# Kernel tuning notes

Hardware: AMD Instinct MI355X
Metric: run time of the kernel (lower is better)

The kernel has to match this reference:

```python
import jax, jax.numpy as jnp
import numpy as np

N = 100000
E = 1600000
D = 128  # in_dim == out_dim


def setup_inputs() -> dict:
    key = jax.random.key(0)
    k1, k2, k3, k4, k5 = jax.random.split(key, 5)
    x = jax.random.normal(k1, (N, D), dtype=jnp.float32)
    edge_index = jax.random.randint(k2, (2, E), 0, N, dtype=jnp.int64)
    edge_attr = jax.random.normal(k3, (E, 8), dtype=jnp.float32)
    # nn.Linear(in_dim, out_dim) params: W [out, in], b [out]
    bound = 1.0 / np.sqrt(D)
    W = jax.random.uniform(k4, (D, D), minval=-bound, maxval=bound, dtype=jnp.float32)
    b = jax.random.uniform(k5, (D,), minval=-bound, maxval=bound, dtype=jnp.float32)
    return {"x": x, "edge_index": edge_index, "edge_attr": edge_attr, "W": W, "b": b}


def reference(x, edge_index, edge_attr, W, b):
    row, col = edge_index[0], edge_index[1]
    # gather neighbor features then scatter-add into destination rows
    agg = jax.ops.segment_sum(x[col], row, num_segments=x.shape[0])  # [N, D]
    h = (x + agg) @ W.T + b  # linear
    return jax.nn.silu(h)
```

## Files before the change

kernel.cpp:

```cpp
#include <hip/hip_runtime.h>
#include <math.h>

#define NN 100000
#define NE 1600000
#define DD 128
#define CAP 64

#define NB     64
#define CHUNK  25000
#define NBUCK  800
#define BNODES 125
#define QCAP2  56
#define OVCAP  8192

typedef short bf16x8 __attribute__((ext_vector_type(8)));
typedef float f32x4  __attribute__((ext_vector_type(4)));

__device__ inline float bf2f(unsigned short u) {
    unsigned int v = ((unsigned int)u) << 16;
    return __uint_as_float(v);
}
__device__ inline unsigned short f2bf(float f) {
    unsigned int u = __float_as_uint(f);
    unsigned int r = (u + 0x7FFFu + ((u >> 16) & 1u)) >> 16;
    return (unsigned short)r;
}

__global__ void f2bf_kernel(const float* __restrict__ src,
                            unsigned short* __restrict__ dst, int n4) {
    int i = blockIdx.x * blockDim.x + threadIdx.x;
    if (i >= n4) return;
    float4 v = ((const float4*)src)[i];
    ushort4 o;
    o.x = f2bf(v.x); o.y = f2bf(v.y); o.z = f2bf(v.z); o.w = f2bf(v.w);
    ((ushort4*)dst)[i] = o;
}

__global__ void zero_ovn_kernel(int* ovn) { *ovn = 0; }

__global__ __launch_bounds__(256)
void partition_kernel(const int* __restrict__ eidx,
                      unsigned long long* __restrict__ q,
                      int* __restrict__ qn,
                      unsigned long long* __restrict__ ovf,
                      int* __restrict__ ovn) {
    __shared__ int qc[NBUCK];
    for (int i = threadIdx.x; i < NBUCK; i += 256) qc[i] = 0;
    __syncthreads();
    const int base = blockIdx.x * CHUNK;
    for (int i = threadIdx.x; i < CHUNK; i += 256) {
        const int e = base + i;
        const int r = __builtin_nontemporal_load(&eidx[e]);
        const int c = __builtin_nontemporal_load(&eidx[NE + e]);
        const int b = r / BNODES;
        const int pos = atomicAdd(&qc[b], 1);
        const unsigned long long pk =
            ((unsigned long long)(unsigned)c << 32) | (unsigned)r;
        if (pos < QCAP2) {
            q[((size_t)blockIdx.x * NBUCK + b) * QCAP2 + pos] = pk;
        } else {
            const int op = atomicAdd(ovn, 1);
            if (op < OVCAP) ovf[op] = pk;
        }
    }
    __syncthreads();
    for (int i = threadIdx.x; i < NBUCK; i += 256) {
        int v = qc[i]; if (v > QCAP2) v = QCAP2;
        qn[blockIdx.x * NBUCK + i] = v;
    }
}

__global__ __launch_bounds__(512)
void build_gather_kernel(const unsigned short* __restrict__ x16,
                         const unsigned long long* __restrict__ q,
                         const int* __restrict__ qn,
                         const unsigned long long* __restrict__ ovf,
                         const int* __restrict__ ovn,
                         unsigned short* __restrict__ V16) {
    __shared__ __align__(16) int adj_l[BNODES * CAP];
    __shared__ int cnt_l[BNODES];
    const int g   = blockIdx.x;
    const int lo  = g * BNODES;
    const int tid = threadIdx.x;

    for (int i = tid; i < BNODES; i += 512) cnt_l[i] = 0;
    __syncthreads();

    {
        const int p   = tid >> 3;
        const int sub = tid & 7;
        const int n = qn[p * NBUCK + g];
        const unsigned long long* qq = q + ((size_t)p * NBUCK + g) * QCAP2;
        for (int i = sub; i < n; i += 8) {
            const unsigned long long pk = qq[i];
            const int r = (int)(pk & 0xffffffffu) - lo;
            const int c = (int)(pk >> 32);
            const int pos = atomicAdd(&cnt_l[r], 1);
            if (pos < CAP) adj_l[(r << 6) + pos] = c;
        }
    }
    {
        int n = *ovn; if (n > OVCAP) n = OVCAP;
        for (int i = tid; i < n; i += 512) {
            const unsigned long long pk = ovf[i];
            const int r = (int)(pk & 0xffffffffu) - lo;
            if ((unsigned)r < (unsigned)BNODES) {
                const int c = (int)(pk >> 32);
                const int pos = atomicAdd(&cnt_l[r], 1);
                if (pos < CAP) adj_l[(r << 6) + pos] = c;
            }
        }
    }
    __syncthreads();

    const int lane = tid & 15;
    const bf16x8* xv = (const bf16x8*)x16;
    for (int ni = (tid >> 4); ni < BNODES; ni += 32) {
        const int node = lo + ni;

        bf16x8 s = xv[(size_t)node * 16 + lane];
        float a[8];
        #pragma unroll
        for (int k = 0; k < 8; ++k) a[k] = bf2f((unsigned short)s[k]);

        int deg = cnt_l[ni]; if (deg > CAP) deg = CAP;
        const int* arow = &adj_l[ni << 6];

        for (int d = 0; d < deg; d += 8) {
            const int4 c0 = *(const int4*)&arow[d];
            const int4 c1 = *(const int4*)&arow[d + 4];
            int idx[8] = {c0.x, c0.y, c0.z, c0.w, c1.x, c1.y, c1.z, c1.w};
            float w[8];
            #pragma unroll
            for (int j = 0; j < 8; ++j) {
                const bool live = (d + j) < deg;
                w[j] = live ? 1.f : 0.f;
                if (!live) idx[j] = node;
            }
            bf16x8 t[8];
            #pragma unroll
            for (int j = 0; j < 8; ++j) t[j] = xv[(size_t)idx[j] * 16 + lane];
            #pragma unroll
            for (int j = 0; j < 8; ++j) {
                #pragma unroll
                for (int k = 0; k < 8; ++k)
                    a[k] = fmaf(w[j], bf2f((unsigned short)t[j][k]), a[k]);
            }
        }

        bf16x8 o;
        #pragma unroll
        for (int k = 0; k < 8; ++k) o[k] = (short)f2bf(a[k]);
        ((bf16x8*)V16)[(size_t)node * 16 + lane] = o;
    }
}

__global__ __launch_bounds__(256)
void gemm_mfma_kernel(const unsigned short* __restrict__ V16,
                      const unsigned short* __restrict__ W16,
                      const float* __restrict__ bias,
                      float* __restrict__ out) {
    const int wave = threadIdx.x >> 6;
    const int lane = threadIdx.x & 63;
    const int strip = blockIdx.x * 4 + wave;
    if (strip >= NN / 16) return;
    const int m0 = strip << 4;
    const int r = lane & 15;
    const int q = lane >> 4;

    const bf16x8* Arow = (const bf16x8*)(V16 + (size_t)(m0 + r) * 128);
    bf16x8 a[4];
    #pragma unroll
    for (int kk = 0; kk < 4; ++kk) a[kk] = Arow[kk * 4 + q];

    f32x4 acc[8];
    #pragma unroll
    for (int n = 0; n < 8; ++n) acc[n] = (f32x4){0.f, 0.f, 0.f, 0.f};

    #pragma unroll
    for (int kk = 0; kk < 4; ++kk) {
        #pragma unroll
        for (int n = 0; n < 8; ++n) {
            const bf16x8 b =
                ((const bf16x8*)(W16 + (size_t)(n * 16 + r) * 128))[kk * 4 + q];
            acc[n] = __builtin_amdgcn_mfma_f32_16x16x32_bf16(a[kk], b, acc[n], 0, 0, 0);
        }
    }

    #pragma unroll
    for (int n = 0; n < 8; ++n) {
        const int col = n * 16 + r;
        const float bv = bias[col];
        #pragma unroll
        for (int i = 0; i < 4; ++i) {
            const int row = m0 + q * 4 + i;
            float h = acc[n][i] + bv;
            h = h / (1.f + __expf(-h));
            out[(size_t)row * 128 + col] = h;
        }
    }
}

extern "C" void kernel_launch(void* const* d_in, const int* in_sizes, int n_in,
                              void* d_out, int out_size, void* d_ws, size_t ws_size,
                              hipStream_t stream) {
    const float* x    = (const float*)d_in[0];
    const int*   eidx = (const int*)d_in[1];
    const float* W    = (const float*)d_in[3];
    const float* b    = (const float*)d_in[4];
    float* out = (float*)d_out;

    char* ws = (char*)d_ws;
    int*                qn  = (int*)ws;
    int*                ovn = (int*)(ws + (256u << 10));
    unsigned long long* ovf = (unsigned long long*)(ws + (320u << 10));
    unsigned long long* q   = (unsigned long long*)(ws + (512u << 10));
    unsigned short*     x16 = (unsigned short*)(ws + (26u << 20));
    unsigned short*     V16 = (unsigned short*)(ws + (51u << 20));
    unsigned short*     W16 = (unsigned short*)(ws + (76u << 20));

    zero_ovn_kernel<<<1, 1, 0, stream>>>(ovn);
    partition_kernel<<<NB, 256, 0, stream>>>(eidx, q, qn, ovf, ovn);
    f2bf_kernel<<<(NN * DD / 4 + 255) / 256, 256, 0, stream>>>(x, x16, NN * DD / 4);
    f2bf_kernel<<<(DD * DD / 4 + 255) / 256, 256, 0, stream>>>(W, W16, DD * DD / 4);
    build_gather_kernel<<<NBUCK, 512, 0, stream>>>(x16, q, qn, ovf, ovn, V16);
    gemm_mfma_kernel<<<(NN / 16 + 3) / 4, 256, 0, stream>>>(V16, W16, b, out);
}
```

Before: 311.9 us.

## Fuse neighbor gather with MFMA GEMM via LDS and merge prep kernels

The aggregation result for each 128-node bucket is written into shared memory with an XOR swizzle instead of global memory. The same block then runs the bf16 MFMA linear plus SiLU on it, which removes the V16 global round trip and a separate GEMM launch. The partition and bf16 conversions are merged into a single prep kernel, and the counter reset becomes a memset. Buckets become power-of-two sized so the bucket divide is a shift. This adds per-block GEMM work after the gather, and padded rows in the last bucket feed uninitialized data that is masked at the store.

```diff
diff --git a/kernel.cpp b/kernel.cpp
--- a/kernel.cpp
+++ b/kernel.cpp
@@ -8,9 +8,9 @@
 
 #define NB     64
 #define CHUNK  25000
-#define NBUCK  800
-#define BNODES 125
-#define QCAP2  56
+#define BNODES 128
+#define NBUCK  782
+#define QCAP2  64
 #define OVCAP  8192
 
 typedef short bf16x8 __attribute__((ext_vector_type(8)));
@@ -26,57 +26,72 @@
     return (unsigned short)r;
 }
 
-__global__ void f2bf_kernel(const float* __restrict__ src,
-                            unsigned short* __restrict__ dst, int n4) {
-    int i = blockIdx.x * blockDim.x + threadIdx.x;
-    if (i >= n4) return;
-    float4 v = ((const float4*)src)[i];
-    ushort4 o;
-    o.x = f2bf(v.x); o.y = f2bf(v.y); o.z = f2bf(v.z); o.w = f2bf(v.w);
-    ((ushort4*)dst)[i] = o;
-}
-
-__global__ void zero_ovn_kernel(int* ovn) { *ovn = 0; }
-
 __global__ __launch_bounds__(256)
-void partition_kernel(const int* __restrict__ eidx,
-                      unsigned long long* __restrict__ q,
-                      int* __restrict__ qn,
-                      unsigned long long* __restrict__ ovf,
-                      int* __restrict__ ovn) {
-    __shared__ int qc[NBUCK];
-    for (int i = threadIdx.x; i < NBUCK; i += 256) qc[i] = 0;
-    __syncthreads();
-    const int base = blockIdx.x * CHUNK;
-    for (int i = threadIdx.x; i < CHUNK; i += 256) {
-        const int e = base + i;
-        const int r = __builtin_nontemporal_load(&eidx[e]);
-        const int c = __builtin_nontemporal_load(&eidx[NE + e]);
-        const int b = r / BNODES;
-        const int pos = atomicAdd(&qc[b], 1);
-        const unsigned long long pk =
-            ((unsigned long long)(unsigned)c << 32) | (unsigned)r;
-        if (pos < QCAP2) {
-            q[((size_t)blockIdx.x * NBUCK + b) * QCAP2 + pos] = pk;
-        } else {
-            const int op = atomicAdd(ovn, 1);
-            if (op < OVCAP) ovf[op] = pk;
-        }
-    }
-    __syncthreads();
-    for (int i = threadIdx.x; i < NBUCK; i += 256) {
-        int v = qc[i]; if (v > QCAP2) v = QCAP2;
-        qn[blockIdx.x * NBUCK + i] = v;
+void prep_kernel(const float* __restrict__ x, const float* __restrict__ W,
+                 const int* __restrict__ eidx,
+                 unsigned short* __restrict__ x16,
+                 unsigned short* __restrict__ W16,
+                 unsigned long long* __restrict__ q, int* __restrict__ qn,
+                 unsigned long long* __restrict__ ovf, int* __restrict__ ovn) {
+    const int blk = blockIdx.x;
+    if (blk < NB) {
+        __shared__ int qc[NBUCK];
+        for (int i = threadIdx.x; i < NBUCK; i += 256) qc[i] = 0;
+        __syncthreads();
+        const int base = blk * CHUNK;
+        for (int i = threadIdx.x; i < CHUNK; i += 256) {
+            const int e = base + i;
+            const int r = __builtin_nontemporal_load(&eidx[e]);
+            const int c = __builtin_nontemporal_load(&eidx[NE + e]);
+            const int b = r >> 7;
+            const int pos = atomicAdd(&qc[b], 1);
+            const unsigned long long pk =
+                ((unsigned long long)(unsigned)c << 32) | (unsigned)r;
+            if (pos < QCAP2) {
+                q[((size_t)blk * NBUCK + b) * QCAP2 + pos] = pk;
+            } else {
+                const int op = atomicAdd(ovn, 1);
+                if (op < OVCAP) ovf[op] = pk;
+            }
+        }
+        __syncthreads();
+        for (int i = threadIdx.x; i < NBUCK; i += 256) {
+            int v = qc[i]; if (v > QCAP2) v = QCAP2;
+            qn[blk * NBUCK + i] = v;
+        }
+    } else if (blk < NB + 3125) {
+        const int base = (blk - NB) * 1024;
+        const float4* src = (const float4*)x;
+        ushort4* dst = (ushort4*)x16;
+        #pragma unroll
+        for (int k = 0; k < 4; ++k) {
+            const int i = base + k * 256 + threadIdx.x;
+            float4 v = src[i];
+            ushort4 o;
+            o.x = f2bf(v.x); o.y = f2bf(v.y); o.z = f2bf(v.z); o.w = f2bf(v.w);
+            dst[i] = o;
+        }
+    } else {
+        const float4* src = (const float4*)W;
+        ushort4* dst = (ushort4*)W16;
+        for (int i = threadIdx.x; i < DD * DD / 4; i += 256) {
+            float4 v = src[i];
+            ushort4 o;
+            o.x = f2bf(v.x); o.y = f2bf(v.y); o.z = f2bf(v.z); o.w = f2bf(v.w);
+            dst[i] = o;
+        }
     }
 }
 
 __global__ __launch_bounds__(512)
-void build_gather_kernel(const unsigned short* __restrict__ x16,
-                         const unsigned long long* __restrict__ q,
-                         const int* __restrict__ qn,
-                         const unsigned long long* __restrict__ ovf,
-                         const int* __restrict__ ovn,
-                         unsigned short* __restrict__ V16) {
+void fused_kernel(const unsigned short* __restrict__ x16,
+                  const unsigned short* __restrict__ W16,
+                  const float* __restrict__ bias,
+                  const unsigned long long* __restrict__ q,
+                  const int* __restrict__ qn,
+                  const unsigned long long* __restrict__ ovf,
+                  const int* __restrict__ ovn,
+                  float* __restrict__ out) {
     __shared__ __align__(16) int adj_l[BNODES * CAP];
     __shared__ int cnt_l[BNODES];
     const int g   = blockIdx.x;
@@ -113,90 +128,92 @@
     }
     __syncthreads();
 
-    const int lane = tid & 15;
-    const bf16x8* xv = (const bf16x8*)x16;
-    for (int ni = (tid >> 4); ni < BNODES; ni += 32) {
-        const int node = lo + ni;
-
-        bf16x8 s = xv[(size_t)node * 16 + lane];
-        float a[8];
-        #pragma unroll
-        for (int k = 0; k < 8; ++k) a[k] = bf2f((unsigned short)s[k]);
-
-        int deg = cnt_l[ni]; if (deg > CAP) deg = CAP;
-        const int* arow = &adj_l[ni << 6];
-
-        for (int d = 0; d < deg; d += 8) {
-            const int4 c0 = *(const int4*)&arow[d];
-            const int4 c1 = *(const int4*)&arow[d + 4];
-            int idx[8] = {c0.x, c0.y, c0.z, c0.w, c1.x, c1.y, c1.z, c1.w};
-            float w[8];
+    {
+        const int lane = tid & 15;
+        const bf16x8* xv = (const bf16x8*)x16;
+        for (int ni = tid >> 4; ni < BNODES; ni += 32) {
+            const int node = lo + ni;
+            if (node < NN) {
+                bf16x8 s = xv[(size_t)node * 16 + lane];
+                float a[8];
+                #pragma unroll
+                for (int k = 0; k < 8; ++k) a[k] = bf2f((unsigned short)s[k]);
+
+                int deg = cnt_l[ni]; if (deg > CAP) deg = CAP;
+                const int* arow = &adj_l[ni << 6];
+                for (int d = 0; d < deg; d += 8) {
+                    const int4 c0 = *(const int4*)&arow[d];
+                    const int4 c1 = *(const int4*)&arow[d + 4];
+                    int idx[8] = {c0.x, c0.y, c0.z, c0.w, c1.x, c1.y, c1.z, c1.w};
+                    float w[8];
+                    #pragma unroll
+                    for (int j = 0; j < 8; ++j) {
+                        const bool live = (d + j) < deg;
+                        w[j] = live ? 1.f : 0.f;
+                        if (!live) idx[j] = node;
+                    }
+                    bf16x8 t[8];
+                    #pragma unroll
+                    for (int j = 0; j < 8; ++j) t[j] = xv[(size_t)idx[j] * 16 + lane];
+                    #pragma unroll
+                    for (int j = 0; j < 8; ++j) {
+                        #pragma unroll
+                        for (int k = 0; k < 8; ++k)
+                            a[k] = fmaf(w[j], bf2f((unsigned short)t[j][k]), a[k]);
+                    }
+                }
+                bf16x8 o;
+                #pragma unroll
+                for (int k = 0; k < 8; ++k) o[k] = (short)f2bf(a[k]);
+                const int byte = (ni << 8) + ((lane << 4) ^ ((ni & 7) << 4));
+                *(bf16x8*)((char*)adj_l + byte) = o;
+            }
+        }
+    }
+    __syncthreads();
+
+    {
+        const int wave = tid >> 6;
+        const int lane = tid & 63;
+        const int m0 = wave << 4;
+        const int r  = lane & 15;
+        const int qd = lane >> 4;
+        const int row = m0 + r;
+
+        bf16x8 a[4];
+        #pragma unroll
+        for (int kk = 0; kk < 4; ++kk) {
+            const int byte = (row << 8) + ((((kk * 4 + qd) << 4)) ^ ((row & 7) << 4));
+            a[kk] = *(const bf16x8*)((const char*)adj_l + byte);
+        }
+
+        f32x4 acc[8];
+        #pragma unroll
+        for (int n = 0; n < 8; ++n) acc[n] = (f32x4){0.f, 0.f, 0.f, 0.f};
+
+        #pragma unroll
+        for (int kk = 0; kk < 4; ++kk) {
             #pragma unroll
-            for (int j = 0; j < 8; ++j) {
-                const bool live = (d + j) < deg;
-                w[j] = live ? 1.f : 0.f;
-                if (!live) idx[j] = node;
-            }
-            bf16x8 t[8];
+            for (int n = 0; n < 8; ++n) {
+                const bf16x8 b =
+                    ((const bf16x8*)(W16 + (size_t)(n * 16 + r) * 128))[kk * 4 + qd];
+                acc[n] = __builtin_amdgcn_mfma_f32_16x16x32_bf16(a[kk], b, acc[n], 0, 0, 0);
+            }
+        }
+
+        #pragma unroll
+        for (int n = 0; n < 8; ++n) {
+            const int col = n * 16 + r;
+            const float bv = bias[col];
             #pragma unroll
-            for (int j = 0; j < 8; ++j) t[j] = xv[(size_t)idx[j] * 16 + lane];
-            #pragma unroll
-            for (int j = 0; j < 8; ++j) {
-                #pragma unroll
-                for (int k = 0; k < 8; ++k)
-                    a[k] = fmaf(w[j], bf2f((unsigned short)t[j][k]), a[k]);
-            }
-        }
-
-        bf16x8 o;
-        #pragma unroll
-        for (int k = 0; k < 8; ++k) o[k] = (short)f2bf(a[k]);
-        ((bf16x8*)V16)[(size_t)node * 16 + lane] = o;
-    }
-}
-
-__global__ __launch_bounds__(256)
-void gemm_mfma_kernel(const unsigned short* __restrict__ V16,
-                      const unsigned short* __restrict__ W16,
-                      const float* __restrict__ bias,
-                      float* __restrict__ out) {
-    const int wave = threadIdx.x >> 6;
-    const int lane = threadIdx.x & 63;
-    const int strip = blockIdx.x * 4 + wave;
-    if (strip >= NN / 16) return;
-    const int m0 = strip << 4;
-    const int r = lane & 15;
-    const int q = lane >> 4;
-
-    const bf16x8* Arow = (const bf16x8*)(V16 + (size_t)(m0 + r) * 128);
-    bf16x8 a[4];
-    #pragma unroll
-    for (int kk = 0; kk < 4; ++kk) a[kk] = Arow[kk * 4 + q];
-
-    f32x4 acc[8];
-    #pragma unroll
-    for (int n = 0; n < 8; ++n) acc[n] = (f32x4){0.f, 0.f, 0.f, 0.f};
-
-    #pragma unroll
-    for (int kk = 0; kk < 4; ++kk) {
-        #pragma unroll
-        for (int n = 0; n < 8; ++n) {
-            const bf16x8 b =
-                ((const bf16x8*)(W16 + (size_t)(n * 16 + r) * 128))[kk * 4 + q];
-            acc[n] = __builtin_amdgcn_mfma_f32_16x16x32_bf16(a[kk], b, acc[n], 0, 0, 0);
-        }
-    }
-
-    #pragma unroll
-    for (int n = 0; n < 8; ++n) {
-        const int col = n * 16 + r;
-        const float bv = bias[col];
-        #pragma unroll
-        for (int i = 0; i < 4; ++i) {
-            const int row = m0 + q * 4 + i;
-            float h = acc[n][i] + bv;
-            h = h / (1.f + __expf(-h));
-            out[(size_t)row * 128 + col] = h;
+            for (int i = 0; i < 4; ++i) {
+                const int orow = lo + m0 + qd * 4 + i;
+                if (orow < NN) {
+                    float h = acc[n][i] + bv;
+                    h = h / (1.f + __expf(-h));
+                    out[(size_t)orow * 128 + col] = h;
+                }
+            }
         }
     }
 }
@@ -216,13 +233,10 @@
     unsigned long long* ovf = (unsigned long long*)(ws + (320u << 10));
     unsigned long long* q   = (unsigned long long*)(ws + (512u << 10));
     unsigned short*     x16 = (unsigned short*)(ws + (26u << 20));
-    unsigned short*     V16 = (unsigned short*)(ws + (51u << 20));
-    unsigned short*     W16 = (unsigned short*)(ws + (76u << 20));
-
-    zero_ovn_kernel<<<1, 1, 0, stream>>>(ovn);
-    partition_kernel<<<NB, 256, 0, stream>>>(eidx, q, qn, ovf, ovn);
-    f2bf_kernel<<<(NN * DD / 4 + 255) / 256, 256, 0, stream>>>(x, x16, NN * DD / 4);
-    f2bf_kernel<<<(DD * DD / 4 + 255) / 256, 256, 0, stream>>>(W, W16, DD * DD / 4);
-    build_gather_kernel<<<NBUCK, 512, 0, stream>>>(x16, q, qn, ovf, ovn, V16);
-    gemm_mfma_kernel<<<(NN / 16 + 3) / 4, 256, 0, stream>>>(V16, W16, b, out);
-}
+    unsigned short*     W16 = (unsigned short*)(ws + (52u << 20));
+
+    hipMemsetAsync(ovn, 0, sizeof(int), stream);
+    prep_kernel<<<NB + 3125 + 1, 256, 0, stream>>>(x, W, eidx, x16, W16,
+                                                   q, qn, ovf, ovn);
+    fused_kernel<<<NBUCK, 512, 0, stream>>>(x16, W16, b, q, qn, ovf, ovn, out);
+}
```

After: 296.7 us. 4.9% less time.
